# Optimization experiments

Hardware: AMD Instinct MI355X
Metric: run time of the kernel (lower is better)

The kernel has to match this reference:

```python
import jax, jax.numpy as jnp
import numpy as np

N, D = 8192, 4096
DIM_K = 4096

def setup_inputs() -> dict:
    key0 = jax.random.key(0)
    k1, k2, k3 = jax.random.split(key0, 3)
    return {
        "query": jax.random.normal(k1, (N, D), dtype=jnp.float32),
        "key": jax.random.normal(k2, (D, N), dtype=jnp.float32),
        "value": jax.random.normal(k3, (N, D), dtype=jnp.float32),
    }

def reference(query, key, value):
    # Faithful to the (buggy) torch module: ELEMENTWISE query * key.T,
    # scale by sqrt(dim_k), elementwise * value, softmax over dim=1
    # (F.softmax's implicit dim for a 2D tensor). The mask branch in the
    # original (`if x:`) cannot execute for multi-element tensors, so it
    # is omitted (mask=None path).
    scale = jnp.sqrt(jnp.float32(DIM_K))
    x = (query * key.T) / scale  # [N, D]
    x = x * value                # [N, D]
    return jax.nn.softmax(x, axis=1)
```

## Files before the change

### kernel.cpp

```cpp
#include <hip/hip_runtime.h>
#include <math.h>


static constexpr int NROW = 8192;
static constexpr int D    = 4096;
static constexpr int RPB  = 8;
static constexpr int LSTR = D + 4;
static constexpr int NT   = 16;

#define LDS_BARRIER() asm volatile("s_waitcnt lgkmcnt(0)\n\ts_barrier" ::: "memory")

__global__ __launch_bounds__(512, 2)
void sdp_softmax_kernel(const float* __restrict__ Q,
                        const float* __restrict__ K,
                        const float* __restrict__ V,
                        float* __restrict__ O)
{
    __shared__ float ldsK[RPB * LSTR];

    const int tid  = threadIdx.x;
    const int wv   = tid >> 6;
    const int lane = tid & 63;

    const int nwg = gridDim.x;
    const int cpx = nwg >> 3;
    const int hb  = blockIdx.x;
    const int lb  = (hb & 7) * cpx + (hb >> 3);

    const int row0 = lb * RPB;
    const int r    = row0 + wv;

    const float* qrow = Q + (size_t)r * D;
    const float* vrow = V + (size_t)r * D;
    float*       orow = O + (size_t)r * D;

    const int il = tid & 7;
    const int jg = tid >> 3;
    const float* kbase = K + (size_t)(8 * jg) * NROW + (size_t)row0 + il;
    const float scl = 0.015625f;

    float sa0, sa1, sa2, sa3, sa4, sa5, sa6, sa7;
    float sb0, sb1, sb2, sb3, sb4, sb5, sb6, sb7;

#define LOADB(R, b)                                                           \
    {                                                                         \
        const float* p = kbase + (size_t)(512 * (b)) * NROW;                  \
        R##0 = p[0];                  R##1 = p[NROW];                         \
        R##2 = p[2 * (size_t)NROW];   R##3 = p[3 * (size_t)NROW];             \
        R##4 = p[4 * (size_t)NROW];   R##5 = p[5 * (size_t)NROW];             \
        R##6 = p[6 * (size_t)NROW];   R##7 = p[7 * (size_t)NROW];             \
    }
#define WRITEB(R, b)                                                          \
    {                                                                         \
        float* w = &ldsK[il * LSTR + 512 * (b) + 8 * jg];                     \
        *(float4*)w       = make_float4(R##0, R##1, R##2, R##3);              \
        *(float4*)(w + 4) = make_float4(R##4, R##5, R##6, R##7);              \
    }

    LOADB(sa, 0)
    float4 qS0 = *(const float4*)(qrow + 0 * 256 + 4 * lane);
    float4 vS0 = *(const float4*)(vrow + 0 * 256 + 4 * lane);
    float4 qS1 = *(const float4*)(qrow + 1 * 256 + 4 * lane);
    float4 vS1 = *(const float4*)(vrow + 1 * 256 + 4 * lane);
    float4 qS2 = *(const float4*)(qrow + 2 * 256 + 4 * lane);
    float4 vS2 = *(const float4*)(vrow + 2 * 256 + 4 * lane);
    float4 qS3 = *(const float4*)(qrow + 3 * 256 + 4 * lane);
    float4 vS3 = *(const float4*)(vrow + 3 * 256 + 4 * lane);

    LOADB(sb, 1) WRITEB(sa, 0)
    LOADB(sa, 2) WRITEB(sb, 1)
    LOADB(sb, 3) WRITEB(sa, 2)
    LOADB(sa, 4) WRITEB(sb, 3)
    LOADB(sb, 5) WRITEB(sa, 4)
    LOADB(sa, 6) WRITEB(sb, 5)
    LOADB(sb, 7) WRITEB(sa, 6)
    WRITEB(sb, 7)
#undef LOADB
#undef WRITEB

    LDS_BARRIER();

    float4 kfA = *(const float4*)&ldsK[wv * LSTR + 4 * lane];
    float4 kfB;
    float4 e0, e1, e2, e3, e4, e5, e6, e7,
           e8, e9, e10, e11, e12, e13, e14, e15;
    float s = 0.0f;

#define BODY(t, ET, KC, KN, QS, VS)                                           \
    {                                                                         \
        if ((t) + 1 < NT)                                                     \
            KN = *(const float4*)&ldsK[wv * LSTR + ((t) + 1) * 256 + 4*lane]; \
        const float4 qc = QS, vc = VS;                                        \
        if ((t) + 4 < NT) {                                                   \
            QS = *(const float4*)(qrow + ((t) + 4) * 256 + 4 * lane);         \
            VS = *(const float4*)(vrow + ((t) + 4) * 256 + 4 * lane);         \
        }                                                                     \
        ET.x = __expf(((qc.x * (KC).x) * scl) * vc.x);                        \
        ET.y = __expf(((qc.y * (KC).y) * scl) * vc.y);                        \
        ET.z = __expf(((qc.z * (KC).z) * scl) * vc.z);                        \
        ET.w = __expf(((qc.w * (KC).w) * scl) * vc.w);                        \
        s += ((ET.x + ET.y) + (ET.z + ET.w));                                 \
        __builtin_amdgcn_sched_barrier(0);                                    \
    }

    BODY(0,  e0,  kfA, kfB, qS0, vS0)
    BODY(1,  e1,  kfB, kfA, qS1, vS1)
    BODY(2,  e2,  kfA, kfB, qS2, vS2)
    BODY(3,  e3,  kfB, kfA, qS3, vS3)
    BODY(4,  e4,  kfA, kfB, qS0, vS0)
    BODY(5,  e5,  kfB, kfA, qS1, vS1)
    BODY(6,  e6,  kfA, kfB, qS2, vS2)
    BODY(7,  e7,  kfB, kfA, qS3, vS3)
    BODY(8,  e8,  kfA, kfB, qS0, vS0)
    BODY(9,  e9,  kfB, kfA, qS1, vS1)
    BODY(10, e10, kfA, kfB, qS2, vS2)
    BODY(11, e11, kfB, kfA, qS3, vS3)
    BODY(12, e12, kfA, kfB, qS0, vS0)
    BODY(13, e13, kfB, kfA, qS1, vS1)
    BODY(14, e14, kfA, kfB, qS2, vS2)
    BODY(15, e15, kfB, kfA, qS3, vS3)
#undef BODY

    #pragma unroll
    for (int i = 1; i < 64; i <<= 1)
        s += __shfl_xor(s, i, 64);
    const float inv = 1.0f / s;

#define WRITE_TILE(t, ET)                                                     \
    {                                                                         \
        float4 xx = ET;                                                       \
        xx.x *= inv; xx.y *= inv; xx.z *= inv; xx.w *= inv;                   \
        *(float4*)(orow + (size_t)(t) * 256 + 4 * lane) = xx;                 \
    }

    WRITE_TILE(0,  e0)  WRITE_TILE(1,  e1)  WRITE_TILE(2,  e2)  WRITE_TILE(3,  e3)
    WRITE_TILE(4,  e4)  WRITE_TILE(5,  e5)  WRITE_TILE(6,  e6)  WRITE_TILE(7,  e7)
    WRITE_TILE(8,  e8)  WRITE_TILE(9,  e9)  WRITE_TILE(10, e10) WRITE_TILE(11, e11)
    WRITE_TILE(12, e12) WRITE_TILE(13, e13) WRITE_TILE(14, e14) WRITE_TILE(15, e15)
#undef WRITE_TILE
}

extern "C" void kernel_launch(void* const* d_in, const int* in_sizes, int n_in,
                              void* d_out, int out_size, void* d_ws, size_t ws_size,
                              hipStream_t stream) {
    const float* Q = (const float*)d_in[0];
    const float* K = (const float*)d_in[1];
    const float* V = (const float*)d_in[2];
    float* O = (float*)d_out;

    dim3 grid(NROW / RPB);
    dim3 block(512);
    sdp_softmax_kernel<<<grid, block, 0, stream>>>(Q, K, V, O);
}
```

Before: 121.3 us.

## Halve LDS tile for K transpose and stream second half mid-compute

The LDS buffer holding the transposed K slice is cut to half the columns. The second half of K is loaded from global memory during the first half's exp computation, then written into the same buffer between two barriers. The aim is to cut LDS per block so more blocks fit per CU (launch bounds raised to 4 blocks), and to overlap the K transpose loads with compute. In exchange the kernel gains an extra barrier pair, more live registers for the prefetched K values, and loses the double-buffered LDS read prefetch.

```diff
diff --git a/kernel.cpp b/kernel.cpp
--- a/kernel.cpp
+++ b/kernel.cpp
@@ -5,12 +5,13 @@
 static constexpr int NROW = 8192;
 static constexpr int D    = 4096;
 static constexpr int RPB  = 8;
-static constexpr int LSTR = D + 4;
+static constexpr int HALF = 2048;
+static constexpr int LSTR = HALF + 4;
 static constexpr int NT   = 16;
 
 #define LDS_BARRIER() asm volatile("s_waitcnt lgkmcnt(0)\n\ts_barrier" ::: "memory")
 
-__global__ __launch_bounds__(512, 2)
+__global__ __launch_bounds__(512, 4)
 void sdp_softmax_kernel(const float* __restrict__ Q,
                         const float* __restrict__ K,
                         const float* __restrict__ V,
@@ -41,85 +42,93 @@
 
     float sa0, sa1, sa2, sa3, sa4, sa5, sa6, sa7;
     float sb0, sb1, sb2, sb3, sb4, sb5, sb6, sb7;
+    float sc0, sc1, sc2, sc3, sc4, sc5, sc6, sc7;
+    float sd0, sd1, sd2, sd3, sd4, sd5, sd6, sd7;
 
-#define LOADB(R, b)                                                           \
+#define LOADB(R, J0)                                                          \
     {                                                                         \
-        const float* p = kbase + (size_t)(512 * (b)) * NROW;                  \
+        const float* p = kbase + (size_t)(J0) * NROW;                         \
         R##0 = p[0];                  R##1 = p[NROW];                         \
         R##2 = p[2 * (size_t)NROW];   R##3 = p[3 * (size_t)NROW];             \
         R##4 = p[4 * (size_t)NROW];   R##5 = p[5 * (size_t)NROW];             \
         R##6 = p[6 * (size_t)NROW];   R##7 = p[7 * (size_t)NROW];             \
     }
-#define WRITEB(R, b)                                                          \
+#define WRITEB(R, COL)                                                        \
     {                                                                         \
-        float* w = &ldsK[il * LSTR + 512 * (b) + 8 * jg];                     \
+        float* w = &ldsK[il * LSTR + (COL) + 8 * jg];                         \
         *(float4*)w       = make_float4(R##0, R##1, R##2, R##3);              \
         *(float4*)(w + 4) = make_float4(R##4, R##5, R##6, R##7);              \
     }
 
     LOADB(sa, 0)
-    float4 qS0 = *(const float4*)(qrow + 0 * 256 + 4 * lane);
-    float4 vS0 = *(const float4*)(vrow + 0 * 256 + 4 * lane);
-    float4 qS1 = *(const float4*)(qrow + 1 * 256 + 4 * lane);
-    float4 vS1 = *(const float4*)(vrow + 1 * 256 + 4 * lane);
-    float4 qS2 = *(const float4*)(qrow + 2 * 256 + 4 * lane);
-    float4 vS2 = *(const float4*)(vrow + 2 * 256 + 4 * lane);
-    float4 qS3 = *(const float4*)(qrow + 3 * 256 + 4 * lane);
-    float4 vS3 = *(const float4*)(vrow + 3 * 256 + 4 * lane);
+    float4 qP0 = *(const float4*)(qrow + 0 * 256 + 4 * lane);
+    float4 vP0 = *(const float4*)(vrow + 0 * 256 + 4 * lane);
+    float4 qP1 = *(const float4*)(qrow + 1 * 256 + 4 * lane);
+    float4 vP1 = *(const float4*)(vrow + 1 * 256 + 4 * lane);
+    float4 qP2 = *(const float4*)(qrow + 2 * 256 + 4 * lane);
+    float4 vP2 = *(const float4*)(vrow + 2 * 256 + 4 * lane);
+    float4 qP3 = *(const float4*)(qrow + 3 * 256 + 4 * lane);
+    float4 vP3 = *(const float4*)(vrow + 3 * 256 + 4 * lane);
 
-    LOADB(sb, 1) WRITEB(sa, 0)
-    LOADB(sa, 2) WRITEB(sb, 1)
-    LOADB(sb, 3) WRITEB(sa, 2)
-    LOADB(sa, 4) WRITEB(sb, 3)
-    LOADB(sb, 5) WRITEB(sa, 4)
-    LOADB(sa, 6) WRITEB(sb, 5)
-    LOADB(sb, 7) WRITEB(sa, 6)
-    WRITEB(sb, 7)
-#undef LOADB
-#undef WRITEB
+    LOADB(sb, 512)   WRITEB(sa, 0)
+    LOADB(sa, 1024)  WRITEB(sb, 512)
+    LOADB(sb, 1536)  WRITEB(sa, 1024)
+    WRITEB(sb, 1536)
 
     LDS_BARRIER();
 
-    float4 kfA = *(const float4*)&ldsK[wv * LSTR + 4 * lane];
-    float4 kfB;
     float4 e0, e1, e2, e3, e4, e5, e6, e7,
            e8, e9, e10, e11, e12, e13, e14, e15;
     float s = 0.0f;
 
-#define BODY(t, ET, KC, KN, QS, VS)                                           \
+#define BODY(t, ET, QS, VS)                                                   \
     {                                                                         \
-        if ((t) + 1 < NT)                                                     \
-            KN = *(const float4*)&ldsK[wv * LSTR + ((t) + 1) * 256 + 4*lane]; \
         const float4 qc = QS, vc = VS;                                        \
         if ((t) + 4 < NT) {                                                   \
             QS = *(const float4*)(qrow + ((t) + 4) * 256 + 4 * lane);         \
             VS = *(const float4*)(vrow + ((t) + 4) * 256 + 4 * lane);         \
         }                                                                     \
-        ET.x = __expf(((qc.x * (KC).x) * scl) * vc.x);                        \
-        ET.y = __expf(((qc.y * (KC).y) * scl) * vc.y);                        \
-        ET.z = __expf(((qc.z * (KC).z) * scl) * vc.z);                        \
-        ET.w = __expf(((qc.w * (KC).w) * scl) * vc.w);                        \
+        const float4 kf =                                                     \
+            *(const float4*)&ldsK[wv * LSTR + ((t) & 7) * 256 + 4 * lane];    \
+        ET.x = __expf(((qc.x * kf.x) * scl) * vc.x);                          \
+        ET.y = __expf(((qc.y * kf.y) * scl) * vc.y);                          \
+        ET.z = __expf(((qc.z * kf.z) * scl) * vc.z);                          \
+        ET.w = __expf(((qc.w * kf.w) * scl) * vc.w);                          \
         s += ((ET.x + ET.y) + (ET.z + ET.w));                                 \
         __builtin_amdgcn_sched_barrier(0);                                    \
     }
 
-    BODY(0,  e0,  kfA, kfB, qS0, vS0)
-    BODY(1,  e1,  kfB, kfA, qS1, vS1)
-    BODY(2,  e2,  kfA, kfB, qS2, vS2)
-    BODY(3,  e3,  kfB, kfA, qS3, vS3)
-    BODY(4,  e4,  kfA, kfB, qS0, vS0)
-    BODY(5,  e5,  kfB, kfA, qS1, vS1)
-    BODY(6,  e6,  kfA, kfB, qS2, vS2)
-    BODY(7,  e7,  kfB, kfA, qS3, vS3)
-    BODY(8,  e8,  kfA, kfB, qS0, vS0)
-    BODY(9,  e9,  kfB, kfA, qS1, vS1)
-    BODY(10, e10, kfA, kfB, qS2, vS2)
-    BODY(11, e11, kfB, kfA, qS3, vS3)
-    BODY(12, e12, kfA, kfB, qS0, vS0)
-    BODY(13, e13, kfB, kfA, qS1, vS1)
-    BODY(14, e14, kfA, kfB, qS2, vS2)
-    BODY(15, e15, kfB, kfA, qS3, vS3)
+    BODY(0,  e0,  qP0, vP0)
+    BODY(1,  e1,  qP1, vP1)
+    BODY(2,  e2,  qP2, vP2)
+    LOADB(sa, 2048)
+    BODY(3,  e3,  qP3, vP3)
+    BODY(4,  e4,  qP0, vP0)
+    LOADB(sb, 2560)
+    BODY(5,  e5,  qP1, vP1)
+    BODY(6,  e6,  qP2, vP2)
+    LOADB(sc, 3072)
+    BODY(7,  e7,  qP3, vP3)
+    LOADB(sd, 3584)
+
+    LDS_BARRIER();
+    WRITEB(sa, 0)
+    WRITEB(sb, 512)
+    WRITEB(sc, 1024)
+    WRITEB(sd, 1536)
+    LDS_BARRIER();
+
+    BODY(8,  e8,  qP0, vP0)
+    BODY(9,  e9,  qP1, vP1)
+    BODY(10, e10, qP2, vP2)
+    BODY(11, e11, qP3, vP3)
+    BODY(12, e12, qP0, vP0)
+    BODY(13, e13, qP1, vP1)
+    BODY(14, e14, qP2, vP2)
+    BODY(15, e15, qP3, vP3)
 #undef BODY
+#undef LOADB
+#undef WRITEB
 
     #pragma unroll
     for (int i = 1; i < 64; i <<= 1)
```

Result: slower. 127.6 us (+5.1%).
